# Kernel optimization log

Measured on AMD Instinct MI355X. Metric: run time of the kernel, lower is better.

## Reference

```python
import jax, jax.numpy as jnp
import numpy as np

EMBED = 1024
HEADS = 16
HEAD_DIM = EMBED // HEADS
FFN_DIM = 4096
SEQ = 2048
BATCH = 2
EPS = 1e-5


def setup_inputs() -> dict:
    key = jax.random.key(0)
    ks = jax.random.split(key, 13)
    s = lambda n: 1.0 / np.sqrt(n)
    return {
        "x": jax.random.normal(ks[0], (BATCH, SEQ, EMBED), jnp.float32),
        # qkv projection (stored as [in, out])
        "w_qkv": jax.random.normal(ks[1], (EMBED, 3 * EMBED), jnp.float32) * s(EMBED),
        "b_qkv": jax.random.normal(ks[2], (3 * EMBED,), jnp.float32) * 0.02,
        "w_out": jax.random.normal(ks[3], (EMBED, EMBED), jnp.float32) * s(EMBED),
        "b_out": jax.random.normal(ks[4], (EMBED,), jnp.float32) * 0.02,
        # FFN
        "w_up": jax.random.normal(ks[5], (EMBED, FFN_DIM), jnp.float32) * s(EMBED),
        "b_up": jax.random.normal(ks[6], (FFN_DIM,), jnp.float32) * 0.02,
        "w_down": jax.random.normal(ks[7], (FFN_DIM, EMBED), jnp.float32) * s(FFN_DIM),
        "b_down": jax.random.normal(ks[8], (EMBED,), jnp.float32) * 0.02,
        # LayerNorms
        "g1": jnp.ones((EMBED,), jnp.float32),
        "be1": jnp.zeros((EMBED,), jnp.float32),
        "g2": jnp.ones((EMBED,), jnp.float32),
        "be2": jnp.zeros((EMBED,), jnp.float32),
    }


def _layernorm(x, g, b):
    mu = jnp.mean(x, axis=-1, keepdims=True)
    var = jnp.mean(jnp.square(x - mu), axis=-1, keepdims=True)
    return (x - mu) * jax.lax.rsqrt(var + EPS) * g + b


def reference(x, w_qkv, b_qkv, w_out, b_out, w_up, b_up, w_down, b_down, g1, be1, g2, be2):
    B, S, E = x.shape
    qkv = (x @ w_qkv + b_qkv).reshape(B, S, 3, HEADS, HEAD_DIM)
    qkv = jnp.transpose(qkv, (2, 0, 3, 1, 4))
    q, k, v = qkv[0], qkv[1], qkv[2]
    scale = 1.0 / jnp.sqrt(jnp.float32(HEAD_DIM))
    attn = jnp.einsum("bhqd,bhkd->bhqk", q, k) * scale  # [B,H,S,S]
    causal = jnp.tril(jnp.ones((S, S), bool))
    attn = jnp.where(causal, attn, -jnp.inf)
    attn = jax.nn.softmax(attn, axis=-1)
    out = jnp.einsum("bhqk,bhkd->bhqd", attn, v)  # [B,H,S,D]
    out = jnp.transpose(out, (0, 2, 1, 3)).reshape(B, S, E)
    attn_out = out @ w_out + b_out
    x = _layernorm(x + attn_out, g1, be1)
    ffn_out = jax.nn.relu(x @ w_up + b_up) @ w_down + b_down
    return _layernorm(x + ffn_out, g2, be2)
```

## Files before the change

### kernel.cpp

```cpp
#include <hip/hip_runtime.h>
#include <hip/hip_bf16.h>

#define EMBED 1024
#define HEADS 16
#define HDIM 64
#define FFN 4096
#define SEQ 2048
#define BATCH 2
#define MTOT (BATCH*SEQ)
#define QSCALE 0.1803368801111137f

typedef __attribute__((ext_vector_type(8))) short bf16x8;
typedef __attribute__((ext_vector_type(4))) float f32x4;
typedef __attribute__((ext_vector_type(16))) float f32x16;
typedef unsigned short u16;
typedef unsigned int u32;

__device__ __forceinline__ u16 f2bf(float f) {
  union { float f; unsigned u; } v; v.f = f;
  unsigned r = v.u + 0x7FFFu + ((v.u >> 16) & 1u);
  return (u16)(r >> 16);
}

__device__ __forceinline__ void async_ld16(const void* g, void* l) {
  __builtin_amdgcn_global_load_lds((const __attribute__((address_space(1))) void*)g,
                                   (__attribute__((address_space(3))) void*)l,
                                   16, 0, 0);
}

__device__ __forceinline__ void qkv_scatter(u16* qp, u16* kp, u16* vp,
                                            int row, int col, float v) {
  const int which = col >> 10, hh = (col >> 6) & 15, d = col & 63;
  const int bb = row >> 11, ss = row & 2047;
  const int bh = bb * 16 + hh;
  if (which == 0) {
    v *= QSCALE;
    size_t idx = ((((size_t)bh * 64 + (ss >> 5)) * 4 + (d >> 4)) << 9)
               + (((ss & 31) + 32 * ((d >> 3) & 1)) << 3) + (d & 7);
    qp[idx] = f2bf(v);
  } else if (which == 1) {
    size_t idx = ((((size_t)bh * 32 + (ss >> 6)) * 8 + (d >> 4) * 2 + ((ss >> 5) & 1)) << 9)
               + (((ss & 31) + 32 * ((d >> 3) & 1)) << 3) + (d & 7);
    kp[idx] = f2bf(v);
  } else {
    size_t idx = ((((size_t)bh * 32 + (ss >> 6)) * 8 + ((ss & 63) >> 4) * 2 + (d >> 5)) << 9)
               + (((d & 31) + 32 * ((ss >> 3) & 1)) << 3) + (ss & 7);
    vp[idx] = f2bf(v);
  }
}

__global__ __launch_bounds__(256) void k_cvt(const float* __restrict__ in,
                                             u16* __restrict__ out, int n4) {
  int i = blockIdx.x * 256 + threadIdx.x;
  int st = gridDim.x * 256;
  for (; i < n4; i += st) {
    float4 v = ((const float4*)in)[i];
    ushort4 o;
    o.x = f2bf(v.x); o.y = f2bf(v.y); o.z = f2bf(v.z); o.w = f2bf(v.w);
    ((ushort4*)out)[i] = o;
  }
}

__global__ __launch_bounds__(256) void k_tr(const float* __restrict__ w,
                                            u16* __restrict__ wT, int K, int N) {
  __shared__ u16 tile[32][33];
  int n0 = blockIdx.x * 32, k0 = blockIdx.y * 32;
  int tx = threadIdx.x, ty = threadIdx.y;
  #pragma unroll
  for (int i = 0; i < 4; ++i) {
    int k = k0 + ty + i * 8;
    tile[ty + i * 8][tx] = f2bf(w[(size_t)k * N + n0 + tx]);
  }
  __syncthreads();
  #pragma unroll
  for (int i = 0; i < 4; ++i) {
    int n = n0 + ty + i * 8;
    wT[(size_t)n * K + k0 + tx] = tile[tx][ty + i * 8];
  }
}

template <int OMODE, bool RELU>
__global__ __launch_bounds__(512) void k_gemm8(
    const u16* __restrict__ A, const u16* __restrict__ BT,
    const float* __restrict__ bias,
    void* __restrict__ out0, void* __restrict__ out1, void* __restrict__ out2,
    int M, int N, int K, int ldk) {
  __shared__ __align__(16) u16 As[2][2][128 * 64];
  __shared__ __align__(16) u16 Bs[2][2][128 * 64];
  const int tid = threadIdx.x;
  const int lane = tid & 63, g = lane >> 4, li = lane & 15;
  const int wid = tid >> 6, wm = wid >> 2, wn = wid & 3;

  const int gx = gridDim.x;
  const int nwg = gx * gridDim.y;
  const int flat = blockIdx.y * gx + blockIdx.x;
  const int cpx = nwg >> 3;
  const int swz = (flat & 7) * cpx + (flat >> 3);
  const int m0 = (swz / gx) * 256, n0 = (swz % gx) * 256;
  const int kchunk = blockIdx.z * K;

  f32x4 acc[8][4] = {};

  const u16* Ablk = A + (size_t)m0 * ldk + kchunk;
  const u16* Bblk = BT + (size_t)n0 * ldk + kchunk;
  const int trow = tid >> 3;
  const int sc = (tid & 7) ^ (trow & 7);

  auto stageA = [&](int buf, int h, int kt) {
    #pragma unroll
    for (int r = 0; r < 2; ++r)
      async_ld16(Ablk + (size_t)(h * 64 + r * 128 + trow) * ldk + kt + sc * 8,
                 &As[buf][h][0] + r * 4096 + tid * 8);
  };
  auto stageB = [&](int buf, int h, int kt) {
    #pragma unroll
    for (int r = 0; r < 2; ++r) {
      const int p = trow + r * 64;
      async_ld16(Bblk + (size_t)(((p >> 5) << 6) + h * 32 + (p & 31)) * ldk + kt + sc * 8,
                 &Bs[buf][h][0] + r * 4096 + tid * 8);
    }
  };

#define VM4_ asm volatile("s_waitcnt vmcnt(4)" ::: "memory")
#define VM2_ asm volatile("s_waitcnt vmcnt(2)" ::: "memory")
#define VM0_ asm volatile("s_waitcnt vmcnt(0)" ::: "memory")
#define VMN_
#define GP8(IH, JH, VMSTMT, STAGE_STMT) do {                                   \
    bf16x8 a_[4][2], b_[2][2];                                                 \
    _Pragma("unroll")                                                          \
    for (int i2 = 0; i2 < 4; ++i2) {                                           \
      const int pa = wm * 64 + i2 * 16 + li;                                   \
      _Pragma("unroll")                                                        \
      for (int ks = 0; ks < 2; ++ks)                                           \
        a_[i2][ks] = *(const bf16x8*)(&As[cur][IH][0] + pa * 64 +              \
                                      (((ks * 4 + g) ^ (li & 7)) * 8));        \
    }                                                                          \
    _Pragma("unroll")                                                          \
    for (int j2 = 0; j2 < 2; ++j2) {                                           \
      const int pb = wn * 32 + j2 * 16 + li;                                   \
      _Pragma("unroll")                                                        \
      for (int ks = 0; ks < 2; ++ks)                                           \
        b_[j2][ks] = *(const bf16x8*)(&Bs[cur][JH][0] + pb * 64 +              \
                                      (((ks * 4 + g) ^ (li & 7)) * 8));        \
    }                                                                          \
    STAGE_STMT;                                                                \
    VMSTMT;                                                                    \
    __builtin_amdgcn_s_barrier();                                              \
    asm volatile("s_waitcnt lgkmcnt(0)" ::: "memory");                         \
    __builtin_amdgcn_sched_barrier(0);                                         \
    __builtin_amdgcn_s_setprio(1);                                             \
    _Pragma("unroll")                                                          \
    for (int ks = 0; ks < 2; ++ks)                                             \
      _Pragma("unroll")                                                        \
      for (int i2 = 0; i2 < 4; ++i2)                                           \
        _Pragma("unroll")                                                      \
        for (int j2 = 0; j2 < 2; ++j2)                                         \
          acc[IH * 4 + i2][JH * 2 + j2] = __builtin_amdgcn_mfma_f32_16x16x32_bf16( \
              a_[i2][ks], b_[j2][ks], acc[IH * 4 + i2][JH * 2 + j2], 0, 0, 0); \
    __builtin_amdgcn_s_setprio(0);                                             \
    __builtin_amdgcn_s_barrier();                                              \
    asm volatile("" ::: "memory");                                             \
  } while (0)

  stageA(0, 0, 0); stageB(0, 0, 0); stageA(0, 1, 0); stageB(0, 1, 0);
  VM4_;
  __builtin_amdgcn_s_barrier();
  asm volatile("" ::: "memory");

  int cur = 0;
  const int nkt = K >> 6;
  for (int t = 0; t < nkt - 1; ++t) {
    const int kn = (t + 1) * 64;
    GP8(0, 0, VM4_, stageA(cur ^ 1, 0, kn));
    GP8(1, 0, VM4_, stageB(cur ^ 1, 0, kn));
    GP8(0, 1, VMN_, stageA(cur ^ 1, 1, kn));
    GP8(1, 1, VM4_, stageB(cur ^ 1, 1, kn));
    cur ^= 1;
  }
  GP8(0, 0, VM2_, );
  GP8(1, 0, VM0_, );
  GP8(0, 1, VMN_, );
  GP8(1, 1, VMN_, );
#undef GP8
#undef VM4_
#undef VM2_
#undef VM0_
#undef VMN_

  float bcol[4];
  #pragma unroll
  for (int j = 0; j < 4; ++j)
    bcol[j] = (OMODE == 3) ? 0.f : bias[n0 + wn * 64 + j * 16 + li];

  #pragma unroll
  for (int i = 0; i < 8; ++i) {
    #pragma unroll
    for (int j = 0; j < 4; ++j) {
      #pragma unroll
      for (int r = 0; r < 4; ++r) {
        int row = m0 + wm * 128 + i * 16 + g * 4 + r;
        int col = n0 + wn * 64 + j * 16 + li;
        float v = acc[i][j][r] + bcol[j];
        if (RELU) v = fmaxf(v, 0.f);
        if (OMODE == 0) {
          ((u16*)out0)[(size_t)row * N + col] = f2bf(v);
        } else if (OMODE == 3) {
          ((float*)out0)[(size_t)blockIdx.z * M * N + (size_t)row * N + col] = v;
        } else {
          qkv_scatter((u16*)out0, (u16*)out1, (u16*)out2, row, col, v);
        }
      }
    }
  }
}

template <bool RELU>
__global__ __launch_bounds__(512) void k_gemmD(
    const u16* __restrict__ A, const u16* __restrict__ BT,
    const float* __restrict__ bias, float* __restrict__ out,
    int M, int N, int K) {
  __shared__ __align__(16) u16 As[4][2][64 * 64];
  __shared__ __align__(16) u16 Bs[4][2][64 * 64];
  const int tid = threadIdx.x;
  const int lane = tid & 63, g = lane >> 4, li = lane & 15;
  const int wid = tid >> 6, wm = wid >> 2, wn = wid & 3;

  const int gx = gridDim.x;
  const int nwg = gx * gridDim.y;
  const int flat = blockIdx.y * gx + blockIdx.x;
  const int cpx = nwg >> 3;
  const int swz = (flat & 7) * cpx + (flat >> 3);
  const int m0 = (swz / gx) * 128, n0 = (swz % gx) * 128;

  f32x4 acc[4][2] = {};

  const u16* Ablk = A + (size_t)m0 * K;
  const u16* Bblk = BT + (size_t)n0 * K;
  const int p = tid >> 3;
  const int c = (tid & 7) ^ (p & 7);

  auto stageAll = [&](int buf, int kt) {
    {
      const int grow = (p >> 5) * 64 + 0 * 32 + (p & 31);
      async_ld16(Ablk + (size_t)grow * K + kt + c * 8, &As[buf][0][0] + tid * 8);
    }
    {
      const int grow = (p >> 4) * 32 + 0 * 16 + (p & 15);
      async_ld16(Bblk + (size_t)grow * K + kt + c * 8, &Bs[buf][0][0] + tid * 8);
    }
    {
      const int grow = (p >> 4) * 32 + 1 * 16 + (p & 15);
      async_ld16(Bblk + (size_t)grow * K + kt + c * 8, &Bs[buf][1][0] + tid * 8);
    }
    {
      const int grow = (p >> 5) * 64 + 1 * 32 + (p & 31);
      async_ld16(Ablk + (size_t)grow * K + kt + c * 8, &As[buf][1][0] + tid * 8);
    }
  };

#define GATE(n) asm volatile("s_waitcnt vmcnt(" #n ")" ::: "memory")
  stageAll(0, 0);
  stageAll(1, 64);
  GATE(5);
  __builtin_amdgcn_s_barrier();
  asm volatile("" ::: "memory");

  const int nkt = K >> 6;
  const int pa0 = wm * 32 + li, pa1 = wm * 32 + 16 + li;
  const int pb = wn * 16 + li;
  for (int t = 0; t < nkt; ++t) {
    const int buf = t & 3;
    bf16x8 a_[2][2], b_[2][2];
    #pragma unroll
    for (int ks = 0; ks < 2; ++ks) {
      a_[0][ks] = *(const bf16x8*)(&As[buf][0][0] + pa0 * 64 + (((ks * 4 + g) ^ (pa0 & 7)) * 8));
      a_[1][ks] = *(const bf16x8*)(&As[buf][0][0] + pa1 * 64 + (((ks * 4 + g) ^ (pa1 & 7)) * 8));
      b_[0][ks] = *(const bf16x8*)(&Bs[buf][0][0] + pb * 64 + (((ks * 4 + g) ^ (pb & 7)) * 8));
      b_[1][ks] = *(const bf16x8*)(&Bs[buf][1][0] + pb * 64 + (((ks * 4 + g) ^ (pb & 7)) * 8));
    }
    if (t + 2 < nkt) {
      stageAll((t + 2) & 3, (t + 2) * 64);
      GATE(8);
    } else if (t + 1 < nkt) {
      GATE(4);
    } else {
      GATE(0);
    }
    __builtin_amdgcn_s_barrier();
    asm volatile("s_waitcnt lgkmcnt(0)" ::: "memory");
    __builtin_amdgcn_sched_barrier(0);
    __builtin_amdgcn_s_setprio(1);
    #pragma unroll
    for (int ks = 0; ks < 2; ++ks)
      #pragma unroll
      for (int i2l = 0; i2l < 2; ++i2l)
        #pragma unroll
        for (int j2 = 0; j2 < 2; ++j2)
          acc[i2l][j2] = __builtin_amdgcn_mfma_f32_16x16x32_bf16(
              a_[i2l][ks], b_[j2][ks], acc[i2l][j2], 0, 0, 0);
    __builtin_amdgcn_s_setprio(0);
    __builtin_amdgcn_s_barrier();
    asm volatile("" ::: "memory");
    #pragma unroll
    for (int ks = 0; ks < 2; ++ks) {
      a_[0][ks] = *(const bf16x8*)(&As[buf][1][0] + pa0 * 64 + (((ks * 4 + g) ^ (pa0 & 7)) * 8));
      a_[1][ks] = *(const bf16x8*)(&As[buf][1][0] + pa1 * 64 + (((ks * 4 + g) ^ (pa1 & 7)) * 8));
    }
    if (t + 2 < nkt)      GATE(5);
    else if (t + 1 < nkt) GATE(1);
    __builtin_amdgcn_s_barrier();
    asm volatile("s_waitcnt lgkmcnt(0)" ::: "memory");
    __builtin_amdgcn_sched_barrier(0);
    __builtin_amdgcn_s_setprio(1);
    #pragma unroll
    for (int ks = 0; ks < 2; ++ks)
      #pragma unroll
      for (int i2l = 0; i2l < 2; ++i2l)
        #pragma unroll
        for (int j2 = 0; j2 < 2; ++j2)
          acc[2 + i2l][j2] = __builtin_amdgcn_mfma_f32_16x16x32_bf16(
              a_[i2l][ks], b_[j2][ks], acc[2 + i2l][j2], 0, 0, 0);
    __builtin_amdgcn_s_setprio(0);
    __builtin_amdgcn_s_barrier();
    asm volatile("" ::: "memory");
  }
#undef GATE

  float bcol[2];
  #pragma unroll
  for (int j = 0; j < 2; ++j) bcol[j] = bias[n0 + wn * 32 + j * 16 + li];

  #pragma unroll
  for (int i = 0; i < 4; ++i) {
    #pragma unroll
    for (int j = 0; j < 2; ++j) {
      #pragma unroll
      for (int r = 0; r < 4; ++r) {
        int row = m0 + wm * 64 + i * 16 + g * 4 + r;
        int col = n0 + wn * 32 + j * 16 + li;
        float v = acc[i][j][r] + bcol[j];
        if (RELU) v = fmaxf(v, 0.f);
        out[(size_t)row * N + col] = v;
      }
    }
  }
}

__global__ __launch_bounds__(256, 3) void k_attn7(
    const u16* __restrict__ Qp, const u16* __restrict__ Kp,
    const u16* __restrict__ Vp, u16* __restrict__ ctx) {
  const int bh = blockIdx.x;
  const int t32 = 63 - (int)blockIdx.y;
  const int b = bh >> 4, h = bh & 15;
  const int tid = threadIdx.x;
  const int wid = tid >> 6, lane = tid & 63;
  const int ql = lane & 31, hl = lane >> 5;

  __shared__ __align__(16) float mrg[3][64][34];

  const int wq0 = t32 * 32;
  const int qg = wq0 + ql;
  const int nt = ((wq0 + 31) >> 6) + 1;

  bf16x8 qf[4];
  {
    const u16* qpb = Qp + ((((size_t)bh * 64 + t32) * 4) << 9) + lane * 8;
    #pragma unroll
    for (int d4 = 0; d4 < 4; ++d4)
      qf[d4] = *(const bf16x8*)(qpb + (d4 << 9));
  }

  const u16* kbase = Kp + (((size_t)bh * 32) << 12) + lane * 8;
  const u16* vbase = Vp + (((size_t)bh * 32) << 12) + lane * 8;

  f32x16 o0 = {}, o1 = {};
  float m_run = -1e30f, l_run = 0.f;

  for (int kt = wid; kt < nt; kt += 4) {
    const bool kh1 = (kt * 64 + 32 <= wq0 + 31);
    const bool domask = (kt * 64 + (kh1 ? 63 : 31) > wq0);
    const u16* kb_ = kbase + ((size_t)kt << 12);
    const u16* vb_ = vbase + ((size_t)kt << 12);

    bf16x8 kf0[4], kf1[4];
    #pragma unroll
    for (int d4 = 0; d4 < 4; ++d4) {
      kf0[d4] = *(const bf16x8*)(kb_ + ((d4 * 2 + 0) << 9));
      if (kh1) kf1[d4] = *(const bf16x8*)(kb_ + ((d4 * 2 + 1) << 9));
    }
    bf16x8 vf0[4], vf1[4];
    #pragma unroll
    for (int t = 0; t < 4; ++t)
      if (t < 2 || kh1) {
        vf0[t] = *(const bf16x8*)(vb_ + ((t * 2 + 0) << 9));
        vf1[t] = *(const bf16x8*)(vb_ + ((t * 2 + 1) << 9));
      }

    f32x16 S0 = {}, S1 = {};
    #pragma unroll
    for (int d4 = 0; d4 < 4; ++d4)
      S0 = __builtin_amdgcn_mfma_f32_32x32x16_bf16(kf0[d4], qf[d4], S0, 0, 0, 0);
    if (kh1) {
      #pragma unroll
      for (int d4 = 0; d4 < 4; ++d4)
        S1 = __builtin_amdgcn_mfma_f32_32x32x16_bf16(kf1[d4], qf[d4], S1, 0, 0, 0);
    }

    if (domask) {
      const int qrel = qg - kt * 64 - 4 * hl;
      #pragma unroll
      for (int r = 0; r < 16; ++r) {
        const int kc = (r & 3) + 8 * (r >> 2);
        S0[r] = (kc <= qrel) ? S0[r] : -3.0e38f;
      }
      if (kh1) {
        #pragma unroll
        for (int r = 0; r < 16; ++r) {
          const int kc = 32 + (r & 3) + 8 * (r >> 2);
          S1[r] = (kc <= qrel) ? S1[r] : -3.0e38f;
        }
      }
    }

    float mt = -3.0e38f;
    #pragma unroll
    for (int r = 0; r < 16; ++r) mt = fmaxf(mt, S0[r]);
    if (kh1) {
      #pragma unroll
      for (int r = 0; r < 16; ++r) mt = fmaxf(mt, S1[r]);
    }
    mt = fmaxf(mt, __shfl_xor(mt, 32, 64));

    if (!__all(mt <= m_run + 8.0f)) {
      const float mn = fmaxf(m_run, mt);
      const float alpha = exp2f(m_run - mn);
      l_run *= alpha;
      o0 *= alpha;
      o1 *= alpha;
      m_run = mn;
    }
    float sum = 0.f;
    #pragma unroll
    for (int r = 0; r < 16; ++r) { S0[r] = exp2f(S0[r] - m_run); sum += S0[r]; }
    if (kh1) {
      #pragma unroll
      for (int r = 0; r < 16; ++r) { S1[r] = exp2f(S1[r] - m_run); sum += S1[r]; }
    }
    sum += __shfl_xor(sum, 32, 64);
    l_run += sum;

    u32 pk[2][8], sw[2][8];
    #pragma unroll
    for (int m = 0; m < 4; ++m) {
      asm("v_cvt_pk_bf16_f32 %0, %1, %2" : "=v"(pk[0][2*m])   : "v"(S0[4*m+0]), "v"(S0[4*m+1]));
      asm("v_cvt_pk_bf16_f32 %0, %1, %2" : "=v"(pk[0][2*m+1]) : "v"(S0[4*m+2]), "v"(S0[4*m+3]));
    }
    #pragma unroll
    for (int i = 0; i < 8; ++i) sw[0][i] = __shfl_xor(pk[0][i], 32, 64);
    if (kh1) {
      #pragma unroll
      for (int m = 0; m < 4; ++m) {
        asm("v_cvt_pk_bf16_f32 %0, %1, %2" : "=v"(pk[1][2*m])   : "v"(S1[4*m+0]), "v"(S1[4*m+1]));
        asm("v_cvt_pk_bf16_f32 %0, %1, %2" : "=v"(pk[1][2*m+1]) : "v"(S1[4*m+2]), "v"(S1[4*m+3]));
      }
      #pragma unroll
      for (int i = 0; i < 8; ++i) sw[1][i] = __shfl_xor(pk[1][i], 32, 64);
    }

    #pragma unroll
    for (int t = 0; t < 4; ++t) {
      if (t < 2 || kh1) {
        const int c = t >> 1, m0 = 2 * (t & 1), m1 = m0 + 1;
        union { u32 u[4]; bf16x8 v; } pf;
        pf.u[0] = hl ? sw[c][2*m1]   : pk[c][2*m0];
        pf.u[1] = hl ? sw[c][2*m1+1] : pk[c][2*m0+1];
        pf.u[2] = hl ? pk[c][2*m1]   : sw[c][2*m0];
        pf.u[3] = hl ? pk[c][2*m1+1] : sw[c][2*m0+1];
        o0 = __builtin_amdgcn_mfma_f32_32x32x16_bf16(vf0[t], pf.v, o0, 0, 0, 0);
        o1 = __builtin_amdgcn_mfma_f32_32x32x16_bf16(vf1[t], pf.v, o1, 0, 0, 0);
      }
    }
  }

  if (wid > 0) {
    float* pq = &mrg[wid - 1][lane][0];
    *(f32x16*)(pq) = o0;
    *(f32x16*)(pq + 16) = o1;
    pq[32] = m_run;
    pq[33] = l_run;
  }
  __syncthreads();
  if (wid > 0) return;

  float M = m_run;
  #pragma unroll
  for (int w = 0; w < 3; ++w) M = fmaxf(M, mrg[w][lane][32]);
  const float fa = exp2f(m_run - M);
  f32x16 acc0 = o0 * fa, acc1 = o1 * fa;
  float L = l_run * fa;
  #pragma unroll
  for (int w = 0; w < 3; ++w) {
    const float* pq = &mrg[w][lane][0];
    const float fw = exp2f(pq[32] - M);
    L += pq[33] * fw;
    f32x16 t0 = *(const f32x16*)(pq);
    f32x16 t1 = *(const f32x16*)(pq + 16);
    acc0 += t0 * fw;
    acc1 += t1 * fw;
  }
  const float inv = 1.f / L;

  u16* outp = ctx + (size_t)(b * SEQ + qg) * EMBED + h * HDIM + 4 * hl;
  #pragma unroll
  for (int m = 0; m < 4; ++m) {
    ushort4 s0v, s1v;
    s0v.x = f2bf(acc0[4*m+0] * inv); s0v.y = f2bf(acc0[4*m+1] * inv);
    s0v.z = f2bf(acc0[4*m+2] * inv); s0v.w = f2bf(acc0[4*m+3] * inv);
    *(ushort4*)(outp + 8 * m) = s0v;
    s1v.x = f2bf(acc1[4*m+0] * inv); s1v.y = f2bf(acc1[4*m+1] * inv);
    s1v.z = f2bf(acc1[4*m+2] * inv); s1v.w = f2bf(acc1[4*m+3] * inv);
    *(ushort4*)(outp + 32 + 8 * m) = s1v;
  }
}

__global__ __launch_bounds__(256) void k_add_ln(
    const float* __restrict__ a, const float* __restrict__ bmat,
    const float* __restrict__ gam, const float* __restrict__ bet,
    float* __restrict__ outf, u16* __restrict__ outb) {
  const int row = blockIdx.x;
  const int t = threadIdx.x;
  __shared__ float red[8];
  float4 va = ((const float4*)(a + (size_t)row * EMBED))[t];
  float4 vb = ((const float4*)(bmat + (size_t)row * EMBED))[t];
  float s0 = va.x + vb.x, s1 = va.y + vb.y, s2 = va.z + vb.z, s3 = va.w + vb.w;
  float sum = s0 + s1 + s2 + s3;
  float sq = s0 * s0 + s1 * s1 + s2 * s2 + s3 * s3;
  #pragma unroll
  for (int m = 1; m < 64; m <<= 1) {
    sum += __shfl_xor(sum, m, 64);
    sq += __shfl_xor(sq, m, 64);
  }
  int wid = t >> 6;
  if ((t & 63) == 0) { red[wid] = sum; red[4 + wid] = sq; }
  __syncthreads();
  sum = red[0] + red[1] + red[2] + red[3];
  sq = red[4] + red[5] + red[6] + red[7];
  float mean = sum * (1.f / EMBED);
  float var = sq * (1.f / EMBED) - mean * mean;
  float rstd = rsqrtf(var + 1e-5f);
  float4 gv = ((const float4*)gam)[t], bev = ((const float4*)bet)[t];
  float y0 = (s0 - mean) * rstd * gv.x + bev.x;
  float y1 = (s1 - mean) * rstd * gv.y + bev.y;
  float y2 = (s2 - mean) * rstd * gv.z + bev.z;
  float y3 = (s3 - mean) * rstd * gv.w + bev.w;
  if (outf) {
    float4 o; o.x = y0; o.y = y1; o.z = y2; o.w = y3;
    ((float4*)(outf + (size_t)row * EMBED))[t] = o;
  }
  if (outb) {
    ushort4 ob; ob.x = f2bf(y0); ob.y = f2bf(y1); ob.z = f2bf(y2); ob.w = f2bf(y3);
    ((ushort4*)(outb + (size_t)row * EMBED))[t] = ob;
  }
}

__global__ __launch_bounds__(256) void k_add_ln4(
    const float* __restrict__ a, const float* __restrict__ parts,
    const float* __restrict__ bias,
    const float* __restrict__ gam, const float* __restrict__ bet,
    float* __restrict__ outf) {
  const int row = blockIdx.x;
  const int t = threadIdx.x;
  __shared__ float red[8];
  float4 va = ((const float4*)(a + (size_t)row * EMBED))[t];
  float4 bv = ((const float4*)bias)[t];
  float s0 = va.x + bv.x, s1 = va.y + bv.y, s2 = va.z + bv.z, s3 = va.w + bv.w;
  #pragma unroll
  for (int c = 0; c < 4; ++c) {
    float4 pv = ((const float4*)(parts + (size_t)c * MTOT * EMBED + (size_t)row * EMBED))[t];
    s0 += pv.x; s1 += pv.y; s2 += pv.z; s3 += pv.w;
  }
  float sum = s0 + s1 + s2 + s3;
  float sq = s0 * s0 + s1 * s1 + s2 * s2 + s3 * s3;
  #pragma unroll
  for (int m = 1; m < 64; m <<= 1) {
    sum += __shfl_xor(sum, m, 64);
    sq += __shfl_xor(sq, m, 64);
  }
  int wid = t >> 6;
  if ((t & 63) == 0) { red[wid] = sum; red[4 + wid] = sq; }
  __syncthreads();
  sum = red[0] + red[1] + red[2] + red[3];
  sq = red[4] + red[5] + red[6] + red[7];
  float mean = sum * (1.f / EMBED);
  float var = sq * (1.f / EMBED) - mean * mean;
  float rstd = rsqrtf(var + 1e-5f);
  float4 gv = ((const float4*)gam)[t], bev = ((const float4*)bet)[t];
  float4 o;
  o.x = (s0 - mean) * rstd * gv.x + bev.x;
  o.y = (s1 - mean) * rstd * gv.y + bev.y;
  o.z = (s2 - mean) * rstd * gv.z + bev.z;
  o.w = (s3 - mean) * rstd * gv.w + bev.w;
  ((float4*)(outf + (size_t)row * EMBED))[t] = o;
}

extern "C" void kernel_launch(void* const* d_in, const int* in_sizes, int n_in,
                              void* d_out, int out_size, void* d_ws, size_t ws_size,
                              hipStream_t stream) {
  const float* x      = (const float*)d_in[0];
  const float* w_qkv  = (const float*)d_in[1];
  const float* b_qkv  = (const float*)d_in[2];
  const float* w_out  = (const float*)d_in[3];
  const float* b_out  = (const float*)d_in[4];
  const float* w_up   = (const float*)d_in[5];
  const float* b_up   = (const float*)d_in[6];
  const float* w_down = (const float*)d_in[7];
  const float* b_down = (const float*)d_in[8];
  const float* g1  = (const float*)d_in[9];
  const float* be1 = (const float*)d_in[10];
  const float* g2  = (const float*)d_in[11];
  const float* be2 = (const float*)d_in[12];

  char* ws = (char*)d_ws;
  size_t off = 0;
  auto alloc = [&](size_t bytes) { void* p = ws + off; off += (bytes + 255) & ~(size_t)255; return p; };

  u16* xb     = (u16*)alloc((size_t)MTOT * EMBED * 2);
  u16* wqkvT  = (u16*)alloc((size_t)3 * EMBED * EMBED * 2);
  u16* woutT  = (u16*)alloc((size_t)EMBED * EMBED * 2);
  u16* wupT   = (u16*)alloc((size_t)FFN * EMBED * 2);
  u16* wdownT = (u16*)alloc((size_t)EMBED * FFN * 2);
  u16* qp     = (u16*)alloc((size_t)MTOT * EMBED * 2);
  u16* kp     = (u16*)alloc((size_t)MTOT * EMBED * 2);
  u16* vp     = (u16*)alloc((size_t)MTOT * EMBED * 2);
  u16* ctx    = (u16*)alloc((size_t)MTOT * EMBED * 2);
  float* attn_proj = (float*)alloc((size_t)MTOT * EMBED * 4);
  float* y_f32     = (float*)alloc((size_t)MTOT * EMBED * 4);
  u16* y_bf16      = (u16*)alloc((size_t)MTOT * EMBED * 2);
  u16* hmid        = (u16*)alloc((size_t)MTOT * FFN * 2);
  float* fparts    = (float*)alloc((size_t)4 * MTOT * EMBED * 4);

  dim3 trb(32, 8);
  k_cvt<<<2048, 256, 0, stream>>>(x, xb, MTOT * EMBED / 4);
  k_tr<<<dim3(3 * EMBED / 32, EMBED / 32), trb, 0, stream>>>(w_qkv, wqkvT, EMBED, 3 * EMBED);
  k_tr<<<dim3(EMBED / 32, EMBED / 32), trb, 0, stream>>>(w_out, woutT, EMBED, EMBED);
  k_tr<<<dim3(FFN / 32, EMBED / 32), trb, 0, stream>>>(w_up, wupT, EMBED, FFN);
  k_tr<<<dim3(EMBED / 32, FFN / 32), trb, 0, stream>>>(w_down, wdownT, FFN, EMBED);

  k_gemm8<2, false><<<dim3(3 * EMBED / 256, MTOT / 256), 512, 0, stream>>>(
      xb, wqkvT, b_qkv, qp, kp, vp, MTOT, 3 * EMBED, EMBED, EMBED);

  k_attn7<<<dim3(BATCH * HEADS, 64), 256, 0, stream>>>(qp, kp, vp, ctx);

  k_gemmD<false><<<dim3(EMBED / 128, MTOT / 128), 512, 0, stream>>>(
      ctx, woutT, b_out, attn_proj, MTOT, EMBED, EMBED);

  k_add_ln<<<MTOT, 256, 0, stream>>>(x, attn_proj, g1, be1, y_f32, y_bf16);

  k_gemm8<0, true><<<dim3(FFN / 256, MTOT / 256), 512, 0, stream>>>(
      y_bf16, wupT, b_up, hmid, nullptr, nullptr, MTOT, FFN, EMBED, EMBED);

  k_gemm8<3, false><<<dim3(EMBED / 256, MTOT / 256, 4), 512, 0, stream>>>(
      hmid, wdownT, nullptr, fparts, nullptr, nullptr, MTOT, EMBED, FFN / 4, FFN);

  k_add_ln4<<<MTOT, 256, 0, stream>>>(y_f32, fparts, b_down, g2, be2, (float*)d_out);

  (void)in_sizes; (void)n_in; (void)out_size; (void)ws_size;
}
```

Before: 240.5 us.

## Restructure GEMM k-loop into two half-phases and drop trailing barriers

```diff
diff --git a/kernel.cpp b/kernel.cpp
--- a/kernel.cpp
+++ b/kernel.cpp
@@ -121,71 +121,85 @@
     }
   };
 
-#define VM4_ asm volatile("s_waitcnt vmcnt(4)" ::: "memory")
+#define VM8_ asm volatile("s_waitcnt vmcnt(8)" ::: "memory")
 #define VM2_ asm volatile("s_waitcnt vmcnt(2)" ::: "memory")
 #define VM0_ asm volatile("s_waitcnt vmcnt(0)" ::: "memory")
-#define VMN_
-#define GP8(IH, JH, VMSTMT, STAGE_STMT) do {                                   \
-    bf16x8 a_[4][2], b_[2][2];                                                 \
-    _Pragma("unroll")                                                          \
-    for (int i2 = 0; i2 < 4; ++i2) {                                           \
-      const int pa = wm * 64 + i2 * 16 + li;                                   \
-      _Pragma("unroll")                                                        \
-      for (int ks = 0; ks < 2; ++ks)                                           \
-        a_[i2][ks] = *(const bf16x8*)(&As[cur][IH][0] + pa * 64 +              \
-                                      (((ks * 4 + g) ^ (li & 7)) * 8));        \
-    }                                                                          \
-    _Pragma("unroll")                                                          \
-    for (int j2 = 0; j2 < 2; ++j2) {                                           \
-      const int pb = wn * 32 + j2 * 16 + li;                                   \
-      _Pragma("unroll")                                                        \
-      for (int ks = 0; ks < 2; ++ks)                                           \
-        b_[j2][ks] = *(const bf16x8*)(&Bs[cur][JH][0] + pb * 64 +              \
-                                      (((ks * 4 + g) ^ (li & 7)) * 8));        \
-    }                                                                          \
-    STAGE_STMT;                                                                \
-    VMSTMT;                                                                    \
-    __builtin_amdgcn_s_barrier();                                              \
-    asm volatile("s_waitcnt lgkmcnt(0)" ::: "memory");                         \
-    __builtin_amdgcn_sched_barrier(0);                                         \
-    __builtin_amdgcn_s_setprio(1);                                             \
-    _Pragma("unroll")                                                          \
-    for (int ks = 0; ks < 2; ++ks)                                             \
-      _Pragma("unroll")                                                        \
-      for (int i2 = 0; i2 < 4; ++i2)                                           \
-        _Pragma("unroll")                                                      \
-        for (int j2 = 0; j2 < 2; ++j2)                                         \
-          acc[IH * 4 + i2][JH * 2 + j2] = __builtin_amdgcn_mfma_f32_16x16x32_bf16( \
-              a_[i2][ks], b_[j2][ks], acc[IH * 4 + i2][JH * 2 + j2], 0, 0, 0); \
-    __builtin_amdgcn_s_setprio(0);                                             \
-    __builtin_amdgcn_s_barrier();                                              \
-    asm volatile("" ::: "memory");                                             \
-  } while (0)
 
   stageA(0, 0, 0); stageB(0, 0, 0); stageA(0, 1, 0); stageB(0, 1, 0);
-  VM4_;
+  VM2_;
   __builtin_amdgcn_s_barrier();
   asm volatile("" ::: "memory");
 
   int cur = 0;
   const int nkt = K >> 6;
-  for (int t = 0; t < nkt - 1; ++t) {
-    const int kn = (t + 1) * 64;
-    GP8(0, 0, VM4_, stageA(cur ^ 1, 0, kn));
-    GP8(1, 0, VM4_, stageB(cur ^ 1, 0, kn));
-    GP8(0, 1, VMN_, stageA(cur ^ 1, 1, kn));
-    GP8(1, 1, VM4_, stageB(cur ^ 1, 1, kn));
+  bf16x8 a_[8][2], b_[2][2];
+  for (int t = 0; t < nkt; ++t) {
+    #pragma unroll
+    for (int i2 = 0; i2 < 8; ++i2) {
+      const int pa = wm * 64 + (i2 & 3) * 16 + li;
+      #pragma unroll
+      for (int ks = 0; ks < 2; ++ks)
+        a_[i2][ks] = *(const bf16x8*)(&As[cur][i2 >> 2][0] + pa * 64 +
+                                      (((ks * 4 + g) ^ (li & 7)) * 8));
+    }
+    #pragma unroll
+    for (int j2 = 0; j2 < 2; ++j2) {
+      const int pb = wn * 32 + j2 * 16 + li;
+      #pragma unroll
+      for (int ks = 0; ks < 2; ++ks)
+        b_[j2][ks] = *(const bf16x8*)(&Bs[cur][0][0] + pb * 64 +
+                                      (((ks * 4 + g) ^ (li & 7)) * 8));
+    }
+    if (t + 1 < nkt) {
+      const int kn = (t + 1) * 64;
+      stageA(cur ^ 1, 0, kn); stageB(cur ^ 1, 0, kn);
+      stageA(cur ^ 1, 1, kn); stageB(cur ^ 1, 1, kn);
+      VM8_;
+    } else {
+      VM0_;
+    }
+    __builtin_amdgcn_s_barrier();
+    asm volatile("s_waitcnt lgkmcnt(0)" ::: "memory");
+    __builtin_amdgcn_sched_barrier(0);
+    __builtin_amdgcn_s_setprio(1);
+    #pragma unroll
+    for (int ks = 0; ks < 2; ++ks)
+      #pragma unroll
+      for (int i2 = 0; i2 < 8; ++i2)
+        #pragma unroll
+        for (int j2 = 0; j2 < 2; ++j2)
+          acc[i2][j2] = __builtin_amdgcn_mfma_f32_16x16x32_bf16(
+              a_[i2][ks], b_[j2][ks], acc[i2][j2], 0, 0, 0);
+    __builtin_amdgcn_s_setprio(0);
+    asm volatile("" ::: "memory");
+    #pragma unroll
+    for (int j2 = 0; j2 < 2; ++j2) {
+      const int pb = wn * 32 + j2 * 16 + li;
+      #pragma unroll
+      for (int ks = 0; ks < 2; ++ks)
+        b_[j2][ks] = *(const bf16x8*)(&Bs[cur][1][0] + pb * 64 +
+                                      (((ks * 4 + g) ^ (li & 7)) * 8));
+    }
+    if (t + 1 < nkt) VM2_;
+    __builtin_amdgcn_s_barrier();
+    asm volatile("s_waitcnt lgkmcnt(0)" ::: "memory");
+    __builtin_amdgcn_sched_barrier(0);
+    __builtin_amdgcn_s_setprio(1);
+    #pragma unroll
+    for (int ks = 0; ks < 2; ++ks)
+      #pragma unroll
+      for (int i2 = 0; i2 < 8; ++i2)
+        #pragma unroll
+        for (int j2 = 0; j2 < 2; ++j2)
+          acc[i2][2 + j2] = __builtin_amdgcn_mfma_f32_16x16x32_bf16(
+              a_[i2][ks], b_[j2][ks], acc[i2][2 + j2], 0, 0, 0);
+    __builtin_amdgcn_s_setprio(0);
+    asm volatile("" ::: "memory");
     cur ^= 1;
   }
-  GP8(0, 0, VM2_, );
-  GP8(1, 0, VM0_, );
-  GP8(0, 1, VMN_, );
-  GP8(1, 1, VMN_, );
-#undef GP8
-#undef VM4_
+#undef VM8_
 #undef VM2_
 #undef VM0_
-#undef VMN_
 
   float bcol[4];
   #pragma unroll
@@ -299,7 +313,6 @@
           acc[i2l][j2] = __builtin_amdgcn_mfma_f32_16x16x32_bf16(
               a_[i2l][ks], b_[j2][ks], acc[i2l][j2], 0, 0, 0);
     __builtin_amdgcn_s_setprio(0);
-    __builtin_amdgcn_s_barrier();
     asm volatile("" ::: "memory");
     #pragma unroll
     for (int ks = 0; ks < 2; ++ks) {
@@ -321,7 +334,6 @@
           acc[2 + i2l][j2] = __builtin_amdgcn_mfma_f32_16x16x32_bf16(
               a_[i2l][ks], b_[j2][ks], acc[2 + i2l][j2], 0, 0, 0);
     __builtin_amdgcn_s_setprio(0);
-    __builtin_amdgcn_s_barrier();
     asm volatile("" ::: "memory");
   }
 #undef GATE
```

Result: faster. 229.4 us (-4.6%).
